# Kernel tuning notes

Measured on AMD Instinct MI355X. Metric: run time of the kernel, lower is better.

Reference implementation:

```python
import jax, jax.numpy as jnp
import numpy as np

B, LQ, LK, D = 64, 1024, 1024, 64
TEMPERATURE = 8.0  # sqrt(D)


def setup_inputs() -> dict:
    key = jax.random.key(0)
    k1, k2, k3, k4, k5, k6 = jax.random.split(key, 6)
    query = jax.random.normal(k1, (B, LQ, D), dtype=jnp.float32)
    key_t = jax.random.normal(k2, (B, LK, D), dtype=jnp.float32)
    value = jax.random.normal(k3, (B, LK, D), dtype=jnp.float32)
    query_mask = jax.random.uniform(k4, (B, LQ)) > 0.1
    key_mask = jax.random.uniform(k5, (B, LK)) > 0.1
    mask = jax.random.uniform(k6, (B, LQ, LK)) > 0.1
    return {"query": query, "key": key_t, "value": value,
            "query_mask": query_mask, "key_mask": key_mask, "mask": mask}


def reference(query, key, value, query_mask, key_mask, mask):
    # unnormalized score: bmm + scale + key/general masking with -inf
    attn = jnp.einsum('bqd,bkd->bqk', query, key) / TEMPERATURE
    neg_inf = jnp.array(-jnp.inf, dtype=attn.dtype)
    if key_mask is not None:
        attn = jnp.where(key_mask[:, None, :], attn, neg_inf)
    if mask is not None:
        attn = jnp.where(mask, attn, neg_inf)
    # softmax over key dim, then zero out masked queries
    attn = jax.nn.softmax(attn, axis=2)
    if query_mask is not None:
        attn = jnp.where(query_mask[:, :, None], attn, 0.0)
    attn_value = jnp.einsum('bqk,bkd->bqd', attn, value)
    return attn_value, attn
```

## Files before the change

### kernel.cpp

```cpp
#include <hip/hip_runtime.h>
#include <hip/hip_bf16.h>


#define NB   64
#define SLQ  1024
#define SLK  1024
#define DH   64
#define TQ   16
#define TK   64
#define NKT  16
#define KSTR 72
#define VSTR 76

typedef __attribute__((ext_vector_type(4))) float          f32x4;
typedef __attribute__((ext_vector_type(8))) __bf16         bf16x8;
typedef __attribute__((ext_vector_type(8))) unsigned short u16x8;
typedef __attribute__((ext_vector_type(4))) unsigned short u16x4;

__device__ __forceinline__ unsigned short f2bf(float f) {
  union { float f; unsigned u; } c; c.f = f;
  unsigned u = c.u;
  u += 0x7fffu + ((u >> 16) & 1u);
  return (unsigned short)(u >> 16);
}
__device__ __forceinline__ u16x4 cvt4(f32x4 v) {
  u16x4 h; h[0]=f2bf(v[0]); h[1]=f2bf(v[1]); h[2]=f2bf(v[2]); h[3]=f2bf(v[3]);
  return h;
}

__global__ __launch_bounds__(256, 4) void sdpa_fused(
    const float* __restrict__ Q, const float* __restrict__ K,
    const float* __restrict__ V, const int* __restrict__ QM,
    const int* __restrict__ KM, const int* __restrict__ MSK,
    float* __restrict__ OUT_AV, float* __restrict__ OUT_P) {
  const int g    = blockIdx.x;
  const int xcd  = g & 7;
  const int slot = g >> 3;
  const int b    = ((slot >> 6) << 3) | xcd;
  const int q0   = (slot & 63) * TQ;

  const int tid  = threadIdx.x;
  const int wave = tid >> 6;
  const int lane = tid & 63;
  const int col  = lane & 15;
  const int quad = lane >> 4;
  const int gk   = wave * 16 + col;

  __shared__ __align__(16) unsigned short Qs[TQ * KSTR];
  __shared__ __align__(16) unsigned short KV[2][TK * VSTR];
  __shared__ __align__(16) unsigned short Ps[2][TQ * KSTR];
  __shared__ float partM[4][TQ], partL[4][TQ];
  __shared__ float rowM[TQ], rowS[TQ];

  const float* kb = K + (size_t)b * SLK * DH;
  const float* vb = V + (size_t)b * SLK * DH;
  const size_t mbase = ((size_t)b * SLQ + q0) * SLK;

  {
    f32x4 val = ((const f32x4*)(Q + ((size_t)b * SLQ + q0) * DH))[tid];
    *(u16x4*)&Qs[(tid >> 4) * KSTR + ((tid & 15) << 2)] = cvt4(val);
  }

  f32x4 kreg[4];
#pragma unroll
  for (int j = 0; j < 4; ++j) kreg[j] = ((const f32x4*)kb)[tid + 256 * j];
  int km_c = KM[b * SLK + gk];
  int msk_c[4];
#pragma unroll
  for (int r = 0; r < 4; ++r)
    msk_c[r] = MSK[mbase + (size_t)(quad * 4 + r) * SLK + gk];

  __syncthreads();
  const bf16x8 aq0 = __builtin_bit_cast(bf16x8, *(const u16x8*)&Qs[col * KSTR + quad * 8]);
  const bf16x8 aq1 = __builtin_bit_cast(bf16x8, *(const u16x8*)&Qs[col * KSTR + quad * 8 + 32]);

  float sreg[NKT][4];
  float mloc[4] = {-INFINITY, -INFINITY, -INFINITY, -INFINITY};
  float lloc[4] = {0.f, 0.f, 0.f, 0.f};

#pragma unroll
  for (int kt = 0; kt < NKT; ++kt) {
#pragma unroll
    for (int j = 0; j < 4; ++j) {
      int idx = tid + 256 * j;
      *(u16x4*)&KV[kt & 1][(idx >> 4) * KSTR + ((idx & 15) << 2)] = cvt4(kreg[j]);
    }
    __syncthreads();

    int km_n = 0, msk_n[4] = {0, 0, 0, 0};
    if (kt < NKT - 1) {
#pragma unroll
      for (int j = 0; j < 4; ++j)
        kreg[j] = ((const f32x4*)kb)[(kt + 1) * (TK * DH / 4) + tid + 256 * j];
      km_n = KM[b * SLK + (kt + 1) * TK + gk];
#pragma unroll
      for (int r = 0; r < 4; ++r)
        msk_n[r] = MSK[mbase + (size_t)(quad * 4 + r) * SLK + (kt + 1) * TK + gk];
    }

    bf16x8 bk0 = __builtin_bit_cast(bf16x8, *(const u16x8*)&KV[kt & 1][gk * KSTR + quad * 8]);
    bf16x8 bk1 = __builtin_bit_cast(bf16x8, *(const u16x8*)&KV[kt & 1][gk * KSTR + quad * 8 + 32]);
    f32x4 acc = {0.f, 0.f, 0.f, 0.f};
    acc = __builtin_amdgcn_mfma_f32_16x16x32_bf16(aq0, bk0, acc, 0, 0, 0);
    acc = __builtin_amdgcn_mfma_f32_16x16x32_bf16(aq1, bk1, acc, 0, 0, 0);

#pragma unroll
    for (int r = 0; r < 4; ++r) {
      float s = (km_c && msk_c[r]) ? acc[r] * 0.125f : -INFINITY;
      sreg[kt][r] = s;
      float mn = fmaxf(mloc[r], s);
      if (mn != -INFINITY) {
        lloc[r] = lloc[r] * __expf(mloc[r] - mn) + __expf(s - mn);
        mloc[r] = mn;
      }
    }
    km_c = km_n;
#pragma unroll
    for (int r = 0; r < 4; ++r) msk_c[r] = msk_n[r];
  }

  f32x4 vreg[4];
#pragma unroll
  for (int j = 0; j < 4; ++j) vreg[j] = ((const f32x4*)vb)[tid + 256 * j];

#pragma unroll
  for (int r = 0; r < 4; ++r) {
#pragma unroll
    for (int off = 1; off < 16; off <<= 1) {
      float om = __shfl_xor(mloc[r], off, 64);
      float ol = __shfl_xor(lloc[r], off, 64);
      float mn = fmaxf(mloc[r], om);
      if (mn != -INFINITY) {
        lloc[r] = lloc[r] * __expf(mloc[r] - mn) + ol * __expf(om - mn);
        mloc[r] = mn;
      }
    }
  }
  if (col == 0) {
#pragma unroll
    for (int r = 0; r < 4; ++r) {
      partM[wave][quad * 4 + r] = mloc[r];
      partL[wave][quad * 4 + r] = lloc[r];
    }
  }
  __syncthreads();
  if (tid < TQ) {
    float M = -INFINITY, L = 0.f;
#pragma unroll
    for (int w = 0; w < 4; ++w) {
      float m_ = partM[w][tid], l_ = partL[w][tid];
      float mn = fmaxf(M, m_);
      if (mn != -INFINITY) {
        L = L * __expf(M - mn) + l_ * __expf(m_ - mn);
        M = mn;
      }
    }
    rowM[tid] = M;
    rowS[tid] = QM[b * SLQ + q0 + tid] ? (1.f / L) : 0.f;
  }
  __syncthreads();

  float Mr[4], Sr[4];
#pragma unroll
  for (int r = 0; r < 4; ++r) { Mr[r] = rowM[quad * 4 + r]; Sr[r] = rowS[quad * 4 + r]; }

  f32x4 acco = {0.f, 0.f, 0.f, 0.f};
#pragma unroll
  for (int kt = 0; kt < NKT; ++kt) {
#pragma unroll
    for (int j = 0; j < 4; ++j) {
      int idx = tid + 256 * j;
      *(u16x4*)&KV[kt & 1][(idx >> 4) * VSTR + ((idx & 15) << 2)] = cvt4(vreg[j]);
    }
    float p[4];
#pragma unroll
    for (int r = 0; r < 4; ++r) {
      p[r] = __expf(sreg[kt][r] - Mr[r]) * Sr[r];
      Ps[kt & 1][(quad * 4 + r) * KSTR + gk] = f2bf(p[r]);
    }
    __syncthreads();

    if (kt < NKT - 1) {
#pragma unroll
      for (int j = 0; j < 4; ++j)
        vreg[j] = ((const f32x4*)vb)[(kt + 1) * (TK * DH / 4) + tid + 256 * j];
    }

#pragma unroll
    for (int r = 0; r < 4; ++r)
      OUT_P[mbase + (size_t)(quad * 4 + r) * SLK + kt * TK + gk] = p[r];

    bf16x8 ap0 = __builtin_bit_cast(bf16x8, *(const u16x8*)&Ps[kt & 1][col * KSTR + quad * 8]);
    bf16x8 ap1 = __builtin_bit_cast(bf16x8, *(const u16x8*)&Ps[kt & 1][col * KSTR + quad * 8 + 32]);
    u16x8 r0, r1;
#pragma unroll
    for (int j = 0; j < 8; ++j) {
      r0[j] = KV[kt & 1][(quad * 8 + j) * VSTR + gk];
      r1[j] = KV[kt & 1][(quad * 8 + j + 32) * VSTR + gk];
    }
    bf16x8 bv0 = __builtin_bit_cast(bf16x8, r0);
    bf16x8 bv1 = __builtin_bit_cast(bf16x8, r1);
    acco = __builtin_amdgcn_mfma_f32_16x16x32_bf16(ap0, bv0, acco, 0, 0, 0);
    acco = __builtin_amdgcn_mfma_f32_16x16x32_bf16(ap1, bv1, acco, 0, 0, 0);
  }

#pragma unroll
  for (int r = 0; r < 4; ++r)
    OUT_AV[((size_t)b * SLQ + q0 + quad * 4 + r) * DH + gk] = acco[r];
}

extern "C" void kernel_launch(void* const* d_in, const int* in_sizes, int n_in,
                              void* d_out, int out_size, void* d_ws, size_t ws_size,
                              hipStream_t stream) {
  const float* q  = (const float*)d_in[0];
  const float* k  = (const float*)d_in[1];
  const float* v  = (const float*)d_in[2];
  const int*   qm = (const int*)d_in[3];
  const int*   km = (const int*)d_in[4];
  const int*   mk = (const int*)d_in[5];
  float* out_av = (float*)d_out;
  float* out_p  = out_av + (size_t)NB * SLQ * DH;
  sdpa_fused<<<dim3(NB * (SLQ / TQ)), dim3(256), 0, stream>>>(q, k, v, qm, km, mk, out_av, out_p);
}
```

Before: 631.1 us.

## Make each wave own a private K/V slice and drop per-tile block barriers

Each wave now loads and converts only its own 16 key rows into a private LDS region, so the QK loop needs no __syncthreads. In the PV stage each wave computes a partial output over its own keys for all 64 head dims across two K tiles per step, and the four partials are reduced through LDS at the end. Q fragments are loaded directly from global memory into registers instead of going through shared memory. The change removes most block-wide barriers, but raises register pressure (launch bounds lowered from 4 to 3) and adds a final cross-wave reduction.

```diff
diff --git a/kernel.cpp b/kernel.cpp
--- a/kernel.cpp
+++ b/kernel.cpp
@@ -9,34 +9,34 @@
 #define TQ   16
 #define TK   64
 #define NKT  16
-#define KSTR 72
+#define KSTR 80
 #define VSTR 76
+#define PSTR 40
 
 typedef __attribute__((ext_vector_type(4))) float          f32x4;
 typedef __attribute__((ext_vector_type(8))) __bf16         bf16x8;
 typedef __attribute__((ext_vector_type(8))) unsigned short u16x8;
 typedef __attribute__((ext_vector_type(4))) unsigned short u16x4;
 
-__device__ __forceinline__ unsigned short f2bf(float f) {
+static __device__ __forceinline__ unsigned short f2bf(float f) {
   union { float f; unsigned u; } c; c.f = f;
   unsigned u = c.u;
   u += 0x7fffu + ((u >> 16) & 1u);
   return (unsigned short)(u >> 16);
 }
-__device__ __forceinline__ u16x4 cvt4(f32x4 v) {
+static __device__ __forceinline__ u16x4 cvt4(f32x4 v) {
   u16x4 h; h[0]=f2bf(v[0]); h[1]=f2bf(v[1]); h[2]=f2bf(v[2]); h[3]=f2bf(v[3]);
   return h;
 }
 
-__global__ __launch_bounds__(256, 4) void sdpa_fused(
+__global__ __launch_bounds__(256, 3) void sdpa_fused(
     const float* __restrict__ Q, const float* __restrict__ K,
     const float* __restrict__ V, const int* __restrict__ QM,
     const int* __restrict__ KM, const int* __restrict__ MSK,
     float* __restrict__ OUT_AV, float* __restrict__ OUT_P) {
   const int g    = blockIdx.x;
-  const int xcd  = g & 7;
   const int slot = g >> 3;
-  const int b    = ((slot >> 6) << 3) | xcd;
+  const int b    = ((slot >> 6) << 3) | (g & 7);
   const int q0   = (slot & 63) * TQ;
 
   const int tid  = threadIdx.x;
@@ -44,62 +44,69 @@
   const int lane = tid & 63;
   const int col  = lane & 15;
   const int quad = lane >> 4;
-  const int gk   = wave * 16 + col;
-
-  __shared__ __align__(16) unsigned short Qs[TQ * KSTR];
-  __shared__ __align__(16) unsigned short KV[2][TK * VSTR];
-  __shared__ __align__(16) unsigned short Ps[2][TQ * KSTR];
-  __shared__ float partM[4][TQ], partL[4][TQ];
-  __shared__ float rowM[TQ], rowS[TQ];
-
-  const float* kb = K + (size_t)b * SLK * DH;
-  const float* vb = V + (size_t)b * SLK * DH;
+  const int lrow = lane >> 4;
+  const int lc4  = (lane & 15) * 4;
+
+  __shared__ __align__(16) unsigned char RAW[25216];
+  unsigned short* Kw = (unsigned short*)RAW + wave * (16 * KSTR);
+  unsigned short* Vw = (unsigned short*)RAW + wave * (32 * VSTR);
+  float*          Ow = (float*)(RAW + wave * (32 * VSTR * 2));
+  unsigned short* Pw = (unsigned short*)(RAW + 19456) + wave * (16 * PSTR);
+  float* partM = (float*)(RAW + 24576);
+  float* partL = partM + 64;
+  float* rowM  = partL + 64;
+  float* rowS  = rowM + 16;
+
+  const f32x4* kb4 = (const f32x4*)(K + (size_t)b * SLK * DH);
+  const f32x4* vb4 = (const f32x4*)(V + (size_t)b * SLK * DH);
   const size_t mbase = ((size_t)b * SLQ + q0) * SLK;
 
+  const float* qp = Q + ((size_t)b * SLQ + q0 + col) * DH + quad * 8;
+  bf16x8 aq0, aq1;
   {
-    f32x4 val = ((const f32x4*)(Q + ((size_t)b * SLQ + q0) * DH))[tid];
-    *(u16x4*)&Qs[(tid >> 4) * KSTR + ((tid & 15) << 2)] = cvt4(val);
-  }
-
-  f32x4 kreg[4];
-#pragma unroll
-  for (int j = 0; j < 4; ++j) kreg[j] = ((const f32x4*)kb)[tid + 256 * j];
-  int km_c = KM[b * SLK + gk];
-  int msk_c[4];
-#pragma unroll
-  for (int r = 0; r < 4; ++r)
-    msk_c[r] = MSK[mbase + (size_t)(quad * 4 + r) * SLK + gk];
-
-  __syncthreads();
-  const bf16x8 aq0 = __builtin_bit_cast(bf16x8, *(const u16x8*)&Qs[col * KSTR + quad * 8]);
-  const bf16x8 aq1 = __builtin_bit_cast(bf16x8, *(const u16x8*)&Qs[col * KSTR + quad * 8 + 32]);
+    u16x4 a = cvt4(*(const f32x4*)qp),        c = cvt4(*(const f32x4*)(qp + 4));
+    u16x4 d = cvt4(*(const f32x4*)(qp + 32)), e = cvt4(*(const f32x4*)(qp + 36));
+    u16x8 h0, h1;
+#pragma unroll
+    for (int j = 0; j < 4; ++j) { h0[j]=a[j]; h0[j+4]=c[j]; h1[j]=d[j]; h1[j+4]=e[j]; }
+    aq0 = __builtin_bit_cast(bf16x8, h0);
+    aq1 = __builtin_bit_cast(bf16x8, h1);
+  }
 
   float sreg[NKT][4];
   float mloc[4] = {-INFINITY, -INFINITY, -INFINITY, -INFINITY};
   float lloc[4] = {0.f, 0.f, 0.f, 0.f};
 
+  f32x4 kreg[4];
+#pragma unroll
+  for (int j = 0; j < 4; ++j)
+    kreg[j] = kb4[(size_t)(wave * 16 + j * 4 + lrow) * 16 + (lane & 15)];
+  int km_c = KM[b * SLK + wave * 16 + col];
+  int msk_c[4];
+#pragma unroll
+  for (int r = 0; r < 4; ++r)
+    msk_c[r] = MSK[mbase + (size_t)(quad * 4 + r) * SLK + wave * 16 + col];
+
 #pragma unroll
   for (int kt = 0; kt < NKT; ++kt) {
 #pragma unroll
-    for (int j = 0; j < 4; ++j) {
-      int idx = tid + 256 * j;
-      *(u16x4*)&KV[kt & 1][(idx >> 4) * KSTR + ((idx & 15) << 2)] = cvt4(kreg[j]);
-    }
-    __syncthreads();
+    for (int j = 0; j < 4; ++j)
+      *(u16x4*)&Kw[(j * 4 + lrow) * KSTR + lc4] = cvt4(kreg[j]);
 
     int km_n = 0, msk_n[4] = {0, 0, 0, 0};
     if (kt < NKT - 1) {
+      const int brow = (kt + 1) * TK + wave * 16;
 #pragma unroll
       for (int j = 0; j < 4; ++j)
-        kreg[j] = ((const f32x4*)kb)[(kt + 1) * (TK * DH / 4) + tid + 256 * j];
-      km_n = KM[b * SLK + (kt + 1) * TK + gk];
+        kreg[j] = kb4[(size_t)(brow + j * 4 + lrow) * 16 + (lane & 15)];
+      km_n = KM[b * SLK + brow + col];
 #pragma unroll
       for (int r = 0; r < 4; ++r)
-        msk_n[r] = MSK[mbase + (size_t)(quad * 4 + r) * SLK + (kt + 1) * TK + gk];
-    }
-
-    bf16x8 bk0 = __builtin_bit_cast(bf16x8, *(const u16x8*)&KV[kt & 1][gk * KSTR + quad * 8]);
-    bf16x8 bk1 = __builtin_bit_cast(bf16x8, *(const u16x8*)&KV[kt & 1][gk * KSTR + quad * 8 + 32]);
+        msk_n[r] = MSK[mbase + (size_t)(quad * 4 + r) * SLK + brow + col];
+    }
+
+    bf16x8 bk0 = __builtin_bit_cast(bf16x8, *(const u16x8*)&Kw[col * KSTR + quad * 8]);
+    bf16x8 bk1 = __builtin_bit_cast(bf16x8, *(const u16x8*)&Kw[col * KSTR + quad * 8 + 32]);
     f32x4 acc = {0.f, 0.f, 0.f, 0.f};
     acc = __builtin_amdgcn_mfma_f32_16x16x32_bf16(aq0, bk0, acc, 0, 0, 0);
     acc = __builtin_amdgcn_mfma_f32_16x16x32_bf16(aq1, bk1, acc, 0, 0, 0);
@@ -119,9 +126,10 @@
     for (int r = 0; r < 4; ++r) msk_c[r] = msk_n[r];
   }
 
-  f32x4 vreg[4];
-#pragma unroll
-  for (int j = 0; j < 4; ++j) vreg[j] = ((const f32x4*)vb)[tid + 256 * j];
+  f32x4 vreg[8];
+#pragma unroll
+  for (int j = 0; j < 8; ++j)
+    vreg[j] = vb4[(size_t)((j >> 2) * TK + wave * 16 + (j & 3) * 4 + lrow) * 16 + (lane & 15)];
 
 #pragma unroll
   for (int r = 0; r < 4; ++r) {
@@ -139,8 +147,8 @@
   if (col == 0) {
 #pragma unroll
     for (int r = 0; r < 4; ++r) {
-      partM[wave][quad * 4 + r] = mloc[r];
-      partL[wave][quad * 4 + r] = lloc[r];
+      partM[wave * 16 + quad * 4 + r] = mloc[r];
+      partL[wave * 16 + quad * 4 + r] = lloc[r];
     }
   }
   __syncthreads();
@@ -148,7 +156,7 @@
     float M = -INFINITY, L = 0.f;
 #pragma unroll
     for (int w = 0; w < 4; ++w) {
-      float m_ = partM[w][tid], l_ = partL[w][tid];
+      float m_ = partM[w * 16 + tid], l_ = partL[w * 16 + tid];
       float mn = fmaxf(M, m_);
       if (mn != -INFINITY) {
         L = L * __expf(M - mn) + l_ * __expf(m_ - mn);
@@ -164,49 +172,64 @@
 #pragma unroll
   for (int r = 0; r < 4; ++r) { Mr[r] = rowM[quad * 4 + r]; Sr[r] = rowS[quad * 4 + r]; }
 
-  f32x4 acco = {0.f, 0.f, 0.f, 0.f};
-#pragma unroll
-  for (int kt = 0; kt < NKT; ++kt) {
-#pragma unroll
-    for (int j = 0; j < 4; ++j) {
-      int idx = tid + 256 * j;
-      *(u16x4*)&KV[kt & 1][(idx >> 4) * VSTR + ((idx & 15) << 2)] = cvt4(vreg[j]);
-    }
-    float p[4];
-#pragma unroll
-    for (int r = 0; r < 4; ++r) {
-      p[r] = __expf(sreg[kt][r] - Mr[r]) * Sr[r];
-      Ps[kt & 1][(quad * 4 + r) * KSTR + gk] = f2bf(p[r]);
-    }
-    __syncthreads();
-
-    if (kt < NKT - 1) {
-#pragma unroll
-      for (int j = 0; j < 4; ++j)
-        vreg[j] = ((const f32x4*)vb)[(kt + 1) * (TK * DH / 4) + tid + 256 * j];
-    }
-
+  f32x4 acco[4] = {{0.f,0.f,0.f,0.f},{0.f,0.f,0.f,0.f},{0.f,0.f,0.f,0.f},{0.f,0.f,0.f,0.f}};
+#pragma unroll
+  for (int st = 0; st < 8; ++st) {
+    const int kt0 = st * 2, kt1 = st * 2 + 1;
+#pragma unroll
+    for (int j = 0; j < 8; ++j)
+      *(u16x4*)&Vw[(j * 4 + lrow) * VSTR + lc4] = cvt4(vreg[j]);
+
+    float p0[4], p1[4];
+#pragma unroll
+    for (int r = 0; r < 4; ++r) {
+      p0[r] = __expf(sreg[kt0][r] - Mr[r]) * Sr[r];
+      p1[r] = __expf(sreg[kt1][r] - Mr[r]) * Sr[r];
+      Pw[(quad * 4 + r) * PSTR + col]      = f2bf(p0[r]);
+      Pw[(quad * 4 + r) * PSTR + 16 + col] = f2bf(p1[r]);
+    }
+#pragma unroll
+    for (int r = 0; r < 4; ++r) {
+      OUT_P[mbase + (size_t)(quad * 4 + r) * SLK + kt0 * TK + wave * 16 + col] = p0[r];
+      OUT_P[mbase + (size_t)(quad * 4 + r) * SLK + kt1 * TK + wave * 16 + col] = p1[r];
+    }
+
+    if (st < 7) {
+#pragma unroll
+      for (int j = 0; j < 8; ++j)
+        vreg[j] = vb4[(size_t)((st * 2 + 2 + (j >> 2)) * TK + wave * 16 + (j & 3) * 4 + lrow) * 16
+                      + (lane & 15)];
+    }
+
+    bf16x8 ap = __builtin_bit_cast(bf16x8, *(const u16x8*)&Pw[col * PSTR + quad * 8]);
+#pragma unroll
+    for (int n0 = 0; n0 < 4; ++n0) {
+      u16x8 rv;
+#pragma unroll
+      for (int j = 0; j < 8; ++j)
+        rv[j] = Vw[(quad * 8 + j) * VSTR + n0 * 16 + col];
+      acco[n0] = __builtin_amdgcn_mfma_f32_16x16x32_bf16(
+          ap, __builtin_bit_cast(bf16x8, rv), acco[n0], 0, 0, 0);
+    }
+  }
+
+#pragma unroll
+  for (int n0 = 0; n0 < 4; ++n0)
 #pragma unroll
     for (int r = 0; r < 4; ++r)
-      OUT_P[mbase + (size_t)(quad * 4 + r) * SLK + kt * TK + gk] = p[r];
-
-    bf16x8 ap0 = __builtin_bit_cast(bf16x8, *(const u16x8*)&Ps[kt & 1][col * KSTR + quad * 8]);
-    bf16x8 ap1 = __builtin_bit_cast(bf16x8, *(const u16x8*)&Ps[kt & 1][col * KSTR + quad * 8 + 32]);
-    u16x8 r0, r1;
-#pragma unroll
-    for (int j = 0; j < 8; ++j) {
-      r0[j] = KV[kt & 1][(quad * 8 + j) * VSTR + gk];
-      r1[j] = KV[kt & 1][(quad * 8 + j + 32) * VSTR + gk];
-    }
-    bf16x8 bv0 = __builtin_bit_cast(bf16x8, r0);
-    bf16x8 bv1 = __builtin_bit_cast(bf16x8, r1);
-    acco = __builtin_amdgcn_mfma_f32_16x16x32_bf16(ap0, bv0, acco, 0, 0, 0);
-    acco = __builtin_amdgcn_mfma_f32_16x16x32_bf16(ap1, bv1, acco, 0, 0, 0);
-  }
-
-#pragma unroll
-  for (int r = 0; r < 4; ++r)
-    OUT_AV[((size_t)b * SLQ + q0 + quad * 4 + r) * DH + gk] = acco[r];
+      Ow[(quad * 4 + r) * 64 + n0 * 16 + col] = acco[n0][r];
+  __syncthreads();
+  {
+    const int qq = tid >> 4, dd = (tid & 15) * 4;
+    f32x4 s = {0.f, 0.f, 0.f, 0.f};
+#pragma unroll
+    for (int w = 0; w < 4; ++w) {
+      const float* Os = (const float*)(RAW + w * (32 * VSTR * 2));
+      f32x4 t = *(const f32x4*)&Os[qq * 64 + dd];
+      s += t;
+    }
+    *(f32x4*)&OUT_AV[((size_t)b * SLQ + q0 + qq) * DH + dd] = s;
+  }
 }
 
 extern "C" void kernel_launch(void* const* d_in, const int* in_sizes, int n_in,
```

Measured after the change: 591.7 us. 1.07x faster.
